# Performance work log

Measured on AMD Instinct MI355X. Metric: run time of the kernel, lower is better.

Reference implementation:

```python
import jax, jax.numpy as jnp
import numpy as np

N = 100000
E = 3200000
K = 10
ALPHA = 0.1
EPS = 1e-5


def setup_inputs() -> dict:
    key = jax.random.key(0)
    ks = jax.random.split(key, 12)
    x = jax.random.normal(ks[0], (N, 512), dtype=jnp.float32)
    edge_index = jax.random.randint(ks[1], (2, E), 0, N, dtype=jnp.int32)
    w1 = jax.random.normal(ks[2], (128, 512), dtype=jnp.float32) * 0.02
    b1 = jnp.zeros((128,), jnp.float32)
    g1 = jnp.ones((128,), jnp.float32)
    be1 = jnp.zeros((128,), jnp.float32)
    m1 = jax.random.normal(ks[3], (128,), dtype=jnp.float32) * 0.1
    v1 = jax.random.uniform(ks[4], (128,), dtype=jnp.float32, minval=0.5, maxval=1.5)
    w2 = jax.random.normal(ks[5], (128, 128), dtype=jnp.float32) * 0.02
    b2 = jnp.zeros((128,), jnp.float32)
    g2 = jnp.ones((128,), jnp.float32)
    be2 = jnp.zeros((128,), jnp.float32)
    m2 = jax.random.normal(ks[6], (128,), dtype=jnp.float32) * 0.1
    v2 = jax.random.uniform(ks[7], (128,), dtype=jnp.float32, minval=0.5, maxval=1.5)
    w3 = jax.random.normal(ks[8], (3, 128), dtype=jnp.float32) * 0.02
    b3 = jnp.zeros((3,), jnp.float32)
    return dict(x=x, edge_index=edge_index, w1=w1, b1=b1, g1=g1, be1=be1, m1=m1, v1=v1,
                w2=w2, b2=b2, g2=g2, be2=be2, m2=m2, v2=v2, w3=w3, b3=b3)


def _bn(y, g, be, m, v):
    return (y - m) * jax.lax.rsqrt(v + EPS) * g + be


def reference(x, edge_index, w1, b1, g1, be1, m1, v1, w2, b2, g2, be2, m2, v2, w3, b3):
    # MLP (eval mode: BN uses running stats, dropout is identity)
    h = jax.nn.relu(_bn(x @ w1.T + b1, g1, be1, m1, v1))
    h = h + jax.nn.relu(_bn(h @ w2.T + b2, g2, be2, m2, v2))
    h = h @ w3.T + b3  # [N, 3]

    # APPNP propagation with GCN normalization + self-loops
    loop = jnp.arange(N, dtype=edge_index.dtype)
    src = jnp.concatenate([edge_index[0], loop])
    dst = jnp.concatenate([edge_index[1], loop])
    deg = jax.ops.segment_sum(jnp.ones_like(src, dtype=h.dtype), dst, num_segments=N)
    dinv = jnp.where(deg > 0, jax.lax.rsqrt(deg), 0.0)
    norm = dinv[src] * dinv[dst]  # [E+N]

    h0 = h
    z = h
    for _ in range(K):
        msg = z[src] * norm[:, None]
        z = jax.ops.segment_sum(msg, dst, num_segments=N)
        z = (1.0 - ALPHA) * z + ALPHA * h0
    return jax.nn.log_softmax(z, axis=1)
```

## Files before the change

kernel.cpp:

```cpp
#include <hip/hip_runtime.h>
#include <cstdint>
#include <cstddef>

#define N_NODES 100000
#define D_IN 512
#define ALPHA 0.1f
#define EPS_BN 1e-5f
#define M_TILE 128
#define BK 64

#define CBITS 8
#define CNODES 256
#define NCBIN 391
#define TILE 8192
#define EPT 32
#define BINCAP 9216

#define NPB 64
#define NB2 1563

typedef float f32x4 __attribute__((ext_vector_type(4)));
typedef __bf16 bf16x8 __attribute__((ext_vector_type(8)));
typedef unsigned short u16x8 __attribute__((ext_vector_type(8)));
typedef unsigned short u16x4 __attribute__((ext_vector_type(4)));

__device__ __forceinline__ unsigned short f2bf(float f) {
  unsigned u = __float_as_uint(f);
  u += 0x7fffu + ((u >> 16) & 1u);
  return (unsigned short)(u >> 16);
}
__device__ __forceinline__ float bf2f(unsigned short h) {
  return __uint_as_float(((unsigned)h) << 16);
}

__global__ void k_prep(const float* __restrict__ w1, const float* __restrict__ b1,
                       const float* __restrict__ g1, const float* __restrict__ be1,
                       const float* __restrict__ m1, const float* __restrict__ v1,
                       const float* __restrict__ w2, const float* __restrict__ b2,
                       const float* __restrict__ g2, const float* __restrict__ be2,
                       const float* __restrict__ m2, const float* __restrict__ v2,
                       unsigned short* __restrict__ w1b, unsigned short* __restrict__ w2b,
                       float* __restrict__ bias1, float* __restrict__ bias2,
                       int* __restrict__ bincur) {
  int idx = blockIdx.x * 256 + threadIdx.x;
  if (idx < 65536) {
    int n = idx >> 9;
    float s = g1[n] * rsqrtf(v1[n] + EPS_BN);
    w1b[idx] = f2bf(w1[idx] * s);
  } else if (idx < 81920) {
    int i = idx - 65536;
    int n = i >> 7;
    float s = g2[n] * rsqrtf(v2[n] + EPS_BN);
    w2b[i] = f2bf(w2[i] * s);
  } else if (idx < 82048) {
    int c = idx - 81920;
    float s = g1[c] * rsqrtf(v1[c] + EPS_BN);
    bias1[c] = (b1[c] - m1[c]) * s + be1[c];
  } else if (idx < 82176) {
    int c = idx - 82048;
    float s = g2[c] * rsqrtf(v2[c] + EPS_BN);
    bias2[c] = (b2[c] - m2[c]) * s + be2[c];
  }
  int bi = idx - 82176;
  if (bi >= 0 && bi < NCBIN) bincur[bi] = 0;
}

#define NB_SCAN 391
__global__ void k_scan2(const int* __restrict__ bincur, int* __restrict__ bsum) {
  __shared__ int s[448];
  int t = threadIdx.x;
  for (int i = t; i < 448; i += 256) s[i] = (i < NB_SCAN) ? bincur[i] : 0;
  __syncthreads();
  if (t < 64) {
    int base = t * 7;
    int vals[7];
    int sum = 0;
#pragma unroll
    for (int j = 0; j < 7; ++j) { vals[j] = s[base + j]; sum += vals[j]; }
    int x = sum;
#pragma unroll
    for (int off = 1; off < 64; off <<= 1) {
      int y = __shfl_up(x, off, 64);
      if (t >= off) x += y;
    }
    int run = x - sum;
#pragma unroll
    for (int j = 0; j < 7; ++j) { int tmp = vals[j]; s[base + j] = run; run += tmp; }
  }
  __syncthreads();
  for (int i = t; i < NB_SCAN; i += 256) bsum[i] = s[i];
}

__global__ void k_scan3(const int* __restrict__ deg, const int* __restrict__ bsum,
                        int* __restrict__ row_start, float* __restrict__ dinv, int E) {
  __shared__ int sb[2][256];
  int t = threadIdx.x;
  int i = blockIdx.x * 256 + t;
  int d = (i < N_NODES) ? deg[i] : 0;
  sb[0][t] = d;
  __syncthreads();
  int cur = 0;
#pragma unroll
  for (int off = 1; off < 256; off <<= 1) {
    int val = sb[cur][t] + ((t >= off) ? sb[cur][t - off] : 0);
    sb[cur ^ 1][t] = val;
    __syncthreads();
    cur ^= 1;
  }
  int incl = sb[cur][t];
  int ex = incl - d;
  if (i < N_NODES) {
    int rs = bsum[blockIdx.x] + ex;
    row_start[i] = rs;
    dinv[i] = rsqrtf((float)(d + 1));
  }
  if (i == N_NODES) row_start[N_NODES] = E;
}

__global__ __launch_bounds__(256) void k_binA(const int* __restrict__ src,
                                              const int* __restrict__ dst, int E,
                                              int* __restrict__ bincur,
                                              unsigned* __restrict__ binned) {
  __shared__ unsigned stage[TILE];
  __shared__ int cnt[NCBIN];
  __shared__ int loff[NCBIN + 1];
  __shared__ int goff[NCBIN];
  __shared__ int sc[2][256];
  const int tid = threadIdx.x;

  for (int i = tid; i < NCBIN; i += 256) cnt[i] = 0;
  __syncthreads();

  const int e0 = blockIdx.x * TILE;
  const int n = min(TILE, E - e0);

  unsigned pk[EPT];
  int bp[EPT];
#pragma unroll
  for (int i = 0; i < EPT; ++i) {
    int o = i * 256 + tid;
    if (o < n) {
      int e = e0 + o;
      int d = dst[e];
      int s = src[e];
      int b = d >> CBITS;
      pk[i] = (unsigned)s | ((unsigned)(d & (CNODES - 1)) << 17);
      int p = atomicAdd(&cnt[b], 1);
      bp[i] = b | (p << 9);
    } else bp[i] = -1;
  }
  __syncthreads();

  int c0 = (2 * tid     < NCBIN) ? cnt[2 * tid]     : 0;
  int c1 = (2 * tid + 1 < NCBIN) ? cnt[2 * tid + 1] : 0;
  sc[0][tid] = c0 + c1;
  __syncthreads();
  int cur = 0;
#pragma unroll
  for (int off = 1; off < 256; off <<= 1) {
    sc[cur ^ 1][tid] = sc[cur][tid] + ((tid >= off) ? sc[cur][tid - off] : 0);
    __syncthreads();
    cur ^= 1;
  }
  int ex = sc[cur][tid] - (c0 + c1);
  if (2 * tid < NCBIN) loff[2 * tid] = ex;
  if (2 * tid + 1 < NCBIN) loff[2 * tid + 1] = ex + c0;
  if (tid == 255) loff[NCBIN] = sc[cur][255];
  __syncthreads();
  for (int i = tid; i < NCBIN; i += 256)
    if (cnt[i] > 0) goff[i] = atomicAdd(&bincur[i], cnt[i]);
  __syncthreads();

#pragma unroll
  for (int i = 0; i < EPT; ++i) {
    if (bp[i] >= 0) {
      int b = bp[i] & 511;
      int p = bp[i] >> 9;
      stage[loff[b] + p] = pk[i];
    }
  }
  __syncthreads();

  for (int i = tid; i < n; i += 256) {
    int lo = 0, hi = NCBIN;
    while (hi - lo > 1) { int mid = (lo + hi) >> 1; if (loff[mid] <= i) lo = mid; else hi = mid; }
    int b = lo;
    binned[(size_t)b * BINCAP + goff[b] + (i - loff[b])] = stage[i];
  }
}

__global__ __launch_bounds__(256) void k_binB1(const unsigned* __restrict__ binned,
                                               const int* __restrict__ bincur,
                                               int* __restrict__ deg) {
  __shared__ int lcnt[CNODES];
  int b = blockIdx.x;
  int t = threadIdx.x;
  lcnt[t] = 0;
  __syncthreads();
  int cnt = bincur[b];
  const unsigned* bp = binned + (size_t)b * BINCAP;
  for (int i = t; i < cnt; i += 256) {
    unsigned v = bp[i];
    atomicAdd(&lcnt[v >> 17], 1);
  }
  __syncthreads();
  int node = (b << CBITS) + t;
  if (node < N_NODES) deg[node] = lcnt[t];
}

__global__ __launch_bounds__(256) void k_binB2(const unsigned* __restrict__ binned,
                                               const int* __restrict__ bincur,
                                               const int* __restrict__ row_start,
                                               unsigned* __restrict__ csr_col) {
  __shared__ unsigned sortbuf[BINCAP];
  __shared__ int lcur[CNODES];
  int b = blockIdx.x;
  int t = threadIdx.x;
  int node0 = b << CBITS;
  int nodes = min(CNODES, N_NODES - node0);
  int rs0 = row_start[node0];
  if (t < nodes) lcur[t] = row_start[node0 + t] - rs0;
  __syncthreads();
  int cnt = bincur[b];
  const unsigned* bp = binned + (size_t)b * BINCAP;
  for (int i = t; i < cnt; i += 256) {
    unsigned v = bp[i];
    int p = atomicAdd(&lcur[v >> 17], 1);
    sortbuf[p] = v & 0x1FFFFu;
  }
  __syncthreads();
  for (int i = t; i < cnt; i += 256) csr_col[rs0 + i] = sortbuf[i];
}

__global__ __launch_bounds__(256, 2) void k_mlp(
    const float* __restrict__ x, const unsigned short* __restrict__ w1b,
    const unsigned short* __restrict__ w2b, const float* __restrict__ bias1,
    const float* __restrict__ bias2, const float* __restrict__ w3,
    const float* __restrict__ b3, const float* __restrict__ dinv,
    float4* __restrict__ h0, float4* __restrict__ zt) {
  __shared__ unsigned short arena[35840];
  __shared__ float lds_w3[384];
  unsigned short* lds_x = arena;
  unsigned short* lds_w = arena + 9216;
  unsigned short* lds_h = arena;
  unsigned short* lds_w2 = arena + 18432;

  const int tid = threadIdx.x;
  const int lane = tid & 63;
  const int wv = tid >> 6;
  const int fr = lane & 15;
  const int kq = (lane >> 4) * 8;
  const int rq = (lane >> 4) * 4;
  const int row0 = blockIdx.x * M_TILE;

  for (int i = tid; i < 384; i += 256) lds_w3[i] = w3[i];

#pragma unroll
  for (int it = 0; it < 8; ++it) {
    int idx = it * 256 + tid;
    int n = idx >> 4, c8 = idx & 15;
    uint4 v = *(const uint4*)(w2b + n * 128 + c8 * 8);
    *(uint4*)(lds_w2 + n * 136 + c8 * 8) = v;
  }

  f32x4 zero4 = {0.f, 0.f, 0.f, 0.f};
  f32x4 acc[2][8];
#pragma unroll
  for (int mt = 0; mt < 2; ++mt)
#pragma unroll
    for (int nt = 0; nt < 8; ++nt) acc[mt][nt] = zero4;

  for (int kb = 0; kb < D_IN; kb += BK) {
#pragma unroll
    for (int it = 0; it < 8; ++it) {
      int idx = it * 256 + tid;
      int r = idx >> 4, c4 = idx & 15;
      int gm = row0 + r;
      if (gm >= N_NODES) gm = N_NODES - 1;
      float4 v = *(const float4*)(x + (size_t)gm * D_IN + kb + c4 * 4);
      u16x4 o;
      o.x = f2bf(v.x); o.y = f2bf(v.y); o.z = f2bf(v.z); o.w = f2bf(v.w);
      *(u16x4*)(lds_x + r * 72 + c4 * 4) = o;
    }
#pragma unroll
    for (int it = 0; it < 4; ++it) {
      int idx = it * 256 + tid;
      int n = idx >> 3, c8 = idx & 7;
      uint4 v = *(const uint4*)(w1b + n * 512 + kb + c8 * 8);
      *(uint4*)(lds_w + n * 72 + c8 * 8) = v;
    }
    __syncthreads();
#pragma unroll
    for (int kk = 0; kk < BK; kk += 32) {
      bf16x8 a[2], b[8];
#pragma unroll
      for (int mt = 0; mt < 2; ++mt)
        a[mt] = __builtin_bit_cast(bf16x8, *(const u16x8*)(lds_x + (wv * 32 + mt * 16 + fr) * 72 + kk + kq));
#pragma unroll
      for (int nt = 0; nt < 8; ++nt)
        b[nt] = __builtin_bit_cast(bf16x8, *(const u16x8*)(lds_w + (nt * 16 + fr) * 72 + kk + kq));
#pragma unroll
      for (int mt = 0; mt < 2; ++mt)
#pragma unroll
        for (int nt = 0; nt < 8; ++nt)
          acc[mt][nt] = __builtin_amdgcn_mfma_f32_16x16x32_bf16(a[mt], b[nt], acc[mt][nt], 0, 0, 0);
    }
    __syncthreads();
  }

  float b1v[8], b2v[8];
#pragma unroll
  for (int nt = 0; nt < 8; ++nt) {
    b1v[nt] = bias1[nt * 16 + fr];
    b2v[nt] = bias2[nt * 16 + fr];
  }
  float hr[2][8][4];
#pragma unroll
  for (int mt = 0; mt < 2; ++mt)
#pragma unroll
    for (int nt = 0; nt < 8; ++nt)
#pragma unroll
      for (int r = 0; r < 4; ++r) {
        int rl = wv * 32 + mt * 16 + rq + r;
        int cl = nt * 16 + fr;
        float h = acc[mt][nt][r] + b1v[nt];
        h = h > 0.f ? h : 0.f;
        hr[mt][nt][r] = h;
        lds_h[rl * 136 + cl] = f2bf(h);
      }
  __syncthreads();

  f32x4 acc2[2][8];
#pragma unroll
  for (int mt = 0; mt < 2; ++mt)
#pragma unroll
    for (int nt = 0; nt < 8; ++nt) acc2[mt][nt] = zero4;
#pragma unroll
  for (int kk = 0; kk < 128; kk += 32) {
    bf16x8 a[2], b[8];
#pragma unroll
    for (int mt = 0; mt < 2; ++mt)
      a[mt] = __builtin_bit_cast(bf16x8, *(const u16x8*)(lds_h + (wv * 32 + mt * 16 + fr) * 136 + kk + kq));
#pragma unroll
    for (int nt = 0; nt < 8; ++nt)
      b[nt] = __builtin_bit_cast(bf16x8, *(const u16x8*)(lds_w2 + (nt * 16 + fr) * 136 + kk + kq));
#pragma unroll
    for (int mt = 0; mt < 2; ++mt)
#pragma unroll
      for (int nt = 0; nt < 8; ++nt)
        acc2[mt][nt] = __builtin_amdgcn_mfma_f32_16x16x32_bf16(a[mt], b[nt], acc2[mt][nt], 0, 0, 0);
  }
  __syncthreads();

#pragma unroll
  for (int mt = 0; mt < 2; ++mt)
#pragma unroll
    for (int nt = 0; nt < 8; ++nt)
#pragma unroll
      for (int r = 0; r < 4; ++r) {
        int rl = wv * 32 + mt * 16 + rq + r;
        int cl = nt * 16 + fr;
        float t2 = acc2[mt][nt][r] + b2v[nt];
        t2 = t2 > 0.f ? t2 : 0.f;
        lds_h[rl * 136 + cl] = f2bf(hr[mt][nt][r] + t2);
      }
  __syncthreads();

  if (tid < 128) {
    int m = tid;
    int gm = row0 + m;
    if (gm < N_NODES) {
      float a0 = 0.f, a1 = 0.f, a2 = 0.f;
#pragma unroll 8
      for (int c = 0; c < 128; ++c) {
        float hv = bf2f(lds_h[m * 136 + c]);
        a0 += hv * lds_w3[c];
        a1 += hv * lds_w3[128 + c];
        a2 += hv * lds_w3[256 + c];
      }
      float z0 = a0 + b3[0], z1 = a1 + b3[1], z2 = a2 + b3[2];
      float di = dinv[gm];
      h0[gm] = make_float4(z0, z1, z2, 0.f);
      zt[gm] = make_float4(di * z0, di * z1, di * z2, 0.f);
    }
  }
}

template <bool FINAL>
__global__ __launch_bounds__(256) void k_iter2(
    const float4* __restrict__ zin, float4* __restrict__ zout,
    const int* __restrict__ row_start, const unsigned* __restrict__ csr_col,
    const float* __restrict__ dinv, const float4* __restrict__ h0v,
    float* __restrict__ out) {
  __shared__ float psum[3][NPB][3];
  const int t = threadIdx.x;
  const int q = t >> 6;
  const int tn = t & 63;
  const int node = blockIdx.x * NPB + tn;
  const bool valid = node < N_NODES;

  int jb = 0, je = 0;
  if (valid) {
    int r0 = row_start[node];
    int r1 = row_start[node + 1];
    int len = r1 - r0;
    jb = r0 + ((len * q) >> 2);
    je = r0 + ((len * (q + 1)) >> 2);
  }

  float sx = 0.f, sy = 0.f, sz = 0.f;
  int j = jb;
  for (; j + 8 <= je; j += 8) {
    unsigned c0 = csr_col[j + 0], c1 = csr_col[j + 1];
    unsigned c2 = csr_col[j + 2], c3 = csr_col[j + 3];
    unsigned c4 = csr_col[j + 4], c5 = csr_col[j + 5];
    unsigned c6 = csr_col[j + 6], c7 = csr_col[j + 7];
    float4 v0 = zin[c0], v1 = zin[c1], v2 = zin[c2], v3 = zin[c3];
    float4 v4 = zin[c4], v5 = zin[c5], v6 = zin[c6], v7 = zin[c7];
    sx += ((v0.x + v1.x) + (v2.x + v3.x)) + ((v4.x + v5.x) + (v6.x + v7.x));
    sy += ((v0.y + v1.y) + (v2.y + v3.y)) + ((v4.y + v5.y) + (v6.y + v7.y));
    sz += ((v0.z + v1.z) + (v2.z + v3.z)) + ((v4.z + v5.z) + (v6.z + v7.z));
  }
  if (j + 4 <= je) {
    unsigned c0 = csr_col[j + 0], c1 = csr_col[j + 1];
    unsigned c2 = csr_col[j + 2], c3 = csr_col[j + 3];
    float4 v0 = zin[c0], v1 = zin[c1], v2 = zin[c2], v3 = zin[c3];
    sx += (v0.x + v1.x) + (v2.x + v3.x);
    sy += (v0.y + v1.y) + (v2.y + v3.y);
    sz += (v0.z + v1.z) + (v2.z + v3.z);
    j += 4;
  }
  if (j + 2 <= je) {
    unsigned c0 = csr_col[j + 0], c1 = csr_col[j + 1];
    float4 v0 = zin[c0], v1 = zin[c1];
    sx += v0.x + v1.x; sy += v0.y + v1.y; sz += v0.z + v1.z;
    j += 2;
  }
  if (j < je) {
    float4 v = zin[csr_col[j]];
    sx += v.x; sy += v.y; sz += v.z;
  }

  if (q) { psum[q - 1][tn][0] = sx; psum[q - 1][tn][1] = sy; psum[q - 1][tn][2] = sz; }
  __syncthreads();
  if (q == 0 && valid) {
    float4 self = zin[node];
    float4 h = h0v[node];
    float di = dinv[node];
    sx += (psum[0][tn][0] + psum[1][tn][0]) + (psum[2][tn][0] + self.x);
    sy += (psum[0][tn][1] + psum[1][tn][1]) + (psum[2][tn][1] + self.y);
    sz += (psum[0][tn][2] + psum[1][tn][2]) + (psum[2][tn][2] + self.z);
    float zx = (1.f - ALPHA) * di * sx + ALPHA * h.x;
    float zy = (1.f - ALPHA) * di * sy + ALPHA * h.y;
    float zz = (1.f - ALPHA) * di * sz + ALPHA * h.z;
    if (!FINAL) {
      zout[node] = make_float4(di * zx, di * zy, di * zz, 0.f);
    } else {
      float mx = fmaxf(zx, fmaxf(zy, zz));
      float l = logf(expf(zx - mx) + expf(zy - mx) + expf(zz - mx));
      out[node * 3 + 0] = zx - mx - l;
      out[node * 3 + 1] = zy - mx - l;
      out[node * 3 + 2] = zz - mx - l;
    }
  }
}

extern "C" void kernel_launch(void* const* d_in, const int* in_sizes, int n_in,
                              void* d_out, int out_size, void* d_ws, size_t ws_size,
                              hipStream_t stream) {
  const float* x   = (const float*)d_in[0];
  const int*   ei  = (const int*)d_in[1];
  const float* w1  = (const float*)d_in[2];
  const float* b1  = (const float*)d_in[3];
  const float* g1  = (const float*)d_in[4];
  const float* be1 = (const float*)d_in[5];
  const float* m1  = (const float*)d_in[6];
  const float* v1  = (const float*)d_in[7];
  const float* w2  = (const float*)d_in[8];
  const float* b2  = (const float*)d_in[9];
  const float* g2  = (const float*)d_in[10];
  const float* be2 = (const float*)d_in[11];
  const float* m2  = (const float*)d_in[12];
  const float* v2  = (const float*)d_in[13];
  const float* w3  = (const float*)d_in[14];
  const float* b3  = (const float*)d_in[15];

  const int E = in_sizes[1] / 2;
  const int* srcA = ei;
  const int* dstA = ei + E;

  char* w = (char*)d_ws;
  size_t off = 0;
  auto alloc = [&](size_t bytes) -> void* {
    void* p = w + off;
    off = (off + bytes + 255) & ~(size_t)255;
    return p;
  };
  unsigned short* w1b   = (unsigned short*)alloc(65536 * 2);
  unsigned short* w2b   = (unsigned short*)alloc(16384 * 2);
  float* bias1          = (float*)alloc(128 * 4);
  float* bias2          = (float*)alloc(128 * 4);
  int*   deg            = (int*)alloc((size_t)N_NODES * 4);
  int*   row_start      = (int*)alloc(((size_t)N_NODES + 1) * 4);
  float* dinv           = (float*)alloc((size_t)N_NODES * 4);
  int*   bsum           = (int*)alloc(512 * 4);
  int*   bincur         = (int*)alloc((size_t)NCBIN * 4);
  float4* h0            = (float4*)alloc((size_t)N_NODES * 16);
  float4* ztA           = (float4*)alloc((size_t)N_NODES * 16);
  float4* ztB           = (float4*)alloc((size_t)N_NODES * 16);
  unsigned* csr_col     = (unsigned*)alloc((size_t)E * 4);
  unsigned* binned      = (unsigned*)alloc((size_t)NCBIN * BINCAP * 4);

  const int NB = (N_NODES + 255) / 256;
  const int NTILE = (E + TILE - 1) / TILE;

  k_prep<<<(82176 + NCBIN + 255) / 256, 256, 0, stream>>>(
      w1, b1, g1, be1, m1, v1, w2, b2, g2, be2, m2, v2, w1b, w2b, bias1, bias2, bincur);
  k_binA<<<NTILE, 256, 0, stream>>>(srcA, dstA, E, bincur, binned);
  k_binB1<<<NCBIN, 256, 0, stream>>>(binned, bincur, deg);
  k_scan2<<<1, 256, 0, stream>>>(bincur, bsum);
  k_scan3<<<NB, 256, 0, stream>>>(deg, bsum, row_start, dinv, E);
  k_binB2<<<NCBIN, 256, 0, stream>>>(binned, bincur, row_start, csr_col);
  k_mlp<<<(N_NODES + M_TILE - 1) / M_TILE, 256, 0, stream>>>(
      x, w1b, w2b, bias1, bias2, w3, b3, dinv, h0, ztA);

  const float4* zin = ztA;
  float4* zout = ztB;
  for (int k = 0; k < 9; ++k) {
    k_iter2<false><<<NB2, 256, 0, stream>>>(zin, zout, row_start, csr_col, dinv, h0, nullptr);
    const float4* tswap = zout;
    zout = (float4*)zin;
    zin = tswap;
  }
  k_iter2<true><<<NB2, 256, 0, stream>>>(zin, nullptr, row_start, csr_col, dinv, h0, (float*)d_out);
}
```

Before: 601.3 us.

## Register-prefetch next x tile in MLP GEMM and stage CSR indices in LDS

The MLP GEMM kernel now loads the next K-slice of x into registers while MFMAs run on the current slice, so global load latency overlaps compute instead of sitting in front of each tile. The propagation kernel first copies the block's contiguous CSR column indices into shared memory with coalesced loads, then gathers neighbor features using those LDS indices. It falls back to global indices when the block's edge count exceeds the LDS capacity. The changes add register pressure, an extra barrier and 12 KB of LDS per block, which may reduce occupancy.

```diff
diff --git a/kernel.cpp b/kernel.cpp
--- a/kernel.cpp
+++ b/kernel.cpp
@@ -18,6 +18,7 @@
 
 #define NPB 64
 #define NB2 1563
+#define LCAP3 3072
 
 typedef float f32x4 __attribute__((ext_vector_type(4)));
 typedef __bf16 bf16x8 __attribute__((ext_vector_type(8)));
@@ -263,6 +264,17 @@
     *(uint4*)(lds_w2 + n * 136 + c8 * 8) = v;
   }
 
+  const int xr_r = 0, xr_c = 0; (void)xr_r; (void)xr_c;
+  f32x4 xr[8];
+#pragma unroll
+  for (int it = 0; it < 8; ++it) {
+    int idx = it * 256 + tid;
+    int r = idx >> 4, c4 = idx & 15;
+    int gm = row0 + r;
+    if (gm >= N_NODES) gm = N_NODES - 1;
+    xr[it] = *(const f32x4*)(x + (size_t)gm * D_IN + 0 + c4 * 4);
+  }
+
   f32x4 zero4 = {0.f, 0.f, 0.f, 0.f};
   f32x4 acc[2][8];
 #pragma unroll
@@ -275,11 +287,8 @@
     for (int it = 0; it < 8; ++it) {
       int idx = it * 256 + tid;
       int r = idx >> 4, c4 = idx & 15;
-      int gm = row0 + r;
-      if (gm >= N_NODES) gm = N_NODES - 1;
-      float4 v = *(const float4*)(x + (size_t)gm * D_IN + kb + c4 * 4);
       u16x4 o;
-      o.x = f2bf(v.x); o.y = f2bf(v.y); o.z = f2bf(v.z); o.w = f2bf(v.w);
+      o.x = f2bf(xr[it].x); o.y = f2bf(xr[it].y); o.z = f2bf(xr[it].z); o.w = f2bf(xr[it].w);
       *(u16x4*)(lds_x + r * 72 + c4 * 4) = o;
     }
 #pragma unroll
@@ -290,6 +299,16 @@
       *(uint4*)(lds_w + n * 72 + c8 * 8) = v;
     }
     __syncthreads();
+    if (kb + BK < D_IN) {
+#pragma unroll
+      for (int it = 0; it < 8; ++it) {
+        int idx = it * 256 + tid;
+        int r = idx >> 4, c4 = idx & 15;
+        int gm = row0 + r;
+        if (gm >= N_NODES) gm = N_NODES - 1;
+        xr[it] = *(const f32x4*)(x + (size_t)gm * D_IN + (kb + BK) + c4 * 4);
+      }
+    }
 #pragma unroll
     for (int kk = 0; kk < BK; kk += 32) {
       bf16x8 a[2], b[8];
@@ -386,18 +405,60 @@
   }
 }
 
+#define GATHER_BODY(IDX)                                                        \
+  for (; j + 8 <= je; j += 8) {                                                 \
+    unsigned c0 = IDX(j + 0), c1 = IDX(j + 1), c2 = IDX(j + 2), c3 = IDX(j + 3);\
+    unsigned c4 = IDX(j + 4), c5 = IDX(j + 5), c6 = IDX(j + 6), c7 = IDX(j + 7);\
+    float4 v0 = zin[c0], v1 = zin[c1], v2 = zin[c2], v3 = zin[c3];              \
+    float4 v4 = zin[c4], v5 = zin[c5], v6 = zin[c6], v7 = zin[c7];              \
+    sx += ((v0.x + v1.x) + (v2.x + v3.x)) + ((v4.x + v5.x) + (v6.x + v7.x));    \
+    sy += ((v0.y + v1.y) + (v2.y + v3.y)) + ((v4.y + v5.y) + (v6.y + v7.y));    \
+    sz += ((v0.z + v1.z) + (v2.z + v3.z)) + ((v4.z + v5.z) + (v6.z + v7.z));    \
+  }                                                                             \
+  if (j + 4 <= je) {                                                            \
+    unsigned c0 = IDX(j + 0), c1 = IDX(j + 1), c2 = IDX(j + 2), c3 = IDX(j + 3);\
+    float4 v0 = zin[c0], v1 = zin[c1], v2 = zin[c2], v3 = zin[c3];              \
+    sx += (v0.x + v1.x) + (v2.x + v3.x);                                        \
+    sy += (v0.y + v1.y) + (v2.y + v3.y);                                        \
+    sz += (v0.z + v1.z) + (v2.z + v3.z);                                        \
+    j += 4;                                                                     \
+  }                                                                             \
+  if (j + 2 <= je) {                                                            \
+    unsigned c0 = IDX(j + 0), c1 = IDX(j + 1);                                  \
+    float4 v0 = zin[c0], v1 = zin[c1];                                          \
+    sx += v0.x + v1.x; sy += v0.y + v1.y; sz += v0.z + v1.z;                    \
+    j += 2;                                                                     \
+  }                                                                             \
+  if (j < je) {                                                                 \
+    float4 v = zin[IDX(j)];                                                     \
+    sx += v.x; sy += v.y; sz += v.z;                                            \
+  }
+
 template <bool FINAL>
 __global__ __launch_bounds__(256) void k_iter2(
     const float4* __restrict__ zin, float4* __restrict__ zout,
     const int* __restrict__ row_start, const unsigned* __restrict__ csr_col,
     const float* __restrict__ dinv, const float4* __restrict__ h0v,
     float* __restrict__ out) {
+  __shared__ unsigned lidx[LCAP3];
   __shared__ float psum[3][NPB][3];
+  __shared__ int srs[2];
   const int t = threadIdx.x;
   const int q = t >> 6;
   const int tn = t & 63;
-  const int node = blockIdx.x * NPB + tn;
+  const int node0 = blockIdx.x * NPB;
+  const int node = node0 + tn;
   const bool valid = node < N_NODES;
+
+  if (t == 0) srs[0] = row_start[node0];
+  if (t == 1) srs[1] = row_start[min(node0 + NPB, N_NODES)];
+  __syncthreads();
+  const int rs0 = srs[0];
+  const int cnt = srs[1] - rs0;
+  const bool use_lds = (cnt <= LCAP3);
+  if (use_lds) {
+    for (int i = t; i < cnt; i += 256) lidx[i] = csr_col[rs0 + i];
+  }
 
   int jb = 0, je = 0;
   if (valid) {
@@ -407,38 +468,20 @@
     jb = r0 + ((len * q) >> 2);
     je = r0 + ((len * (q + 1)) >> 2);
   }
+  __syncthreads();
 
   float sx = 0.f, sy = 0.f, sz = 0.f;
-  int j = jb;
-  for (; j + 8 <= je; j += 8) {
-    unsigned c0 = csr_col[j + 0], c1 = csr_col[j + 1];
-    unsigned c2 = csr_col[j + 2], c3 = csr_col[j + 3];
-    unsigned c4 = csr_col[j + 4], c5 = csr_col[j + 5];
-    unsigned c6 = csr_col[j + 6], c7 = csr_col[j + 7];
-    float4 v0 = zin[c0], v1 = zin[c1], v2 = zin[c2], v3 = zin[c3];
-    float4 v4 = zin[c4], v5 = zin[c5], v6 = zin[c6], v7 = zin[c7];
-    sx += ((v0.x + v1.x) + (v2.x + v3.x)) + ((v4.x + v5.x) + (v6.x + v7.x));
-    sy += ((v0.y + v1.y) + (v2.y + v3.y)) + ((v4.y + v5.y) + (v6.y + v7.y));
-    sz += ((v0.z + v1.z) + (v2.z + v3.z)) + ((v4.z + v5.z) + (v6.z + v7.z));
-  }
-  if (j + 4 <= je) {
-    unsigned c0 = csr_col[j + 0], c1 = csr_col[j + 1];
-    unsigned c2 = csr_col[j + 2], c3 = csr_col[j + 3];
-    float4 v0 = zin[c0], v1 = zin[c1], v2 = zin[c2], v3 = zin[c3];
-    sx += (v0.x + v1.x) + (v2.x + v3.x);
-    sy += (v0.y + v1.y) + (v2.y + v3.y);
-    sz += (v0.z + v1.z) + (v2.z + v3.z);
-    j += 4;
-  }
-  if (j + 2 <= je) {
-    unsigned c0 = csr_col[j + 0], c1 = csr_col[j + 1];
-    float4 v0 = zin[c0], v1 = zin[c1];
-    sx += v0.x + v1.x; sy += v0.y + v1.y; sz += v0.z + v1.z;
-    j += 2;
-  }
-  if (j < je) {
-    float4 v = zin[csr_col[j]];
-    sx += v.x; sy += v.y; sz += v.z;
+  if (use_lds) {
+    int j = jb - rs0;
+    je -= rs0;
+#define IDXL(J) lidx[J]
+    GATHER_BODY(IDXL)
+#undef IDXL
+  } else {
+    int j = jb;
+#define IDXG(J) csr_col[J]
+    GATHER_BODY(IDXG)
+#undef IDXG
   }
 
   if (q) { psum[q - 1][tn][0] = sx; psum[q - 1][tn][1] = sy; psum[q - 1][tn][2] = sz; }
```

Result: no change. 596.5 us (-0.8%).
